# Optimization experiments

Measured on AMD Instinct MI355X. Metric: run time of the kernel, lower is better.

The kernel has to match this reference:

```python
import jax, jax.numpy as jnp
import numpy as np


def setup_inputs() -> dict:
    key = jax.random.key(0)
    k1, k2 = jax.random.split(key)
    b, t_x, d = 16, 1024, 256
    max_dur = 8
    x = jax.random.normal(k1, (b, t_x, d), dtype=jnp.float32)
    repeat_count = jax.random.randint(k2, (b, t_x), 0, max_dur, dtype=jnp.int64)
    out_len = t_x * (max_dur - 1)  # static upper bound on max(cumsum(durations))
    return {"x": x, "repeat_count": repeat_count, "out_len": out_len}


def reference(x, repeat_count, out_len):
    # x: (b, t_x, d); repeat_count: (b, t_x) int; out_len: static int (t_y)
    cum = jnp.cumsum(repeat_count.astype(jnp.int64), axis=1)          # (b, t_x)
    # content mask: M[b, i, j] = 1 if j < cum[b, i]
    cols = jnp.arange(out_len)                                        # (t_y,)
    M = (cols[None, None, :] < cum[:, :, None]).astype(x.dtype)       # (b, t_x, t_y)
    # row-wise diff along t_x turns prefix masks into per-phoneme one-hot spans
    M = jnp.concatenate([M[:, :1, :], M[:, 1:, :] - M[:, :-1, :]], axis=1)
    # bmm(M^T, x): expand phonemes into frames
    out = jnp.einsum('bxt,bxd->btd', M, x)                            # (b, t_y, d)
    lengths = jnp.max(cum, axis=1)                                    # (b,)
    return out, lengths
```

## Files before the change

kernel.cpp:

```cpp
#include <hip/hip_runtime.h>

#define B       16
#define TX      1024
#define D       256
#define OUT_LEN 7168
#define TILE    16

__global__ __launch_bounds__(256) void lr_scan_kernel(
        const int* __restrict__ rc,
        int* __restrict__ cum,
        float* __restrict__ len_out)
{
    __shared__ int part[256];
    const int b = blockIdx.x;
    const int t = threadIdx.x;

    const int4* rc4 = (const int4*)(rc + b * TX);
    int4 v = rc4[t];
    const int s0 = v.x;
    const int s1 = s0 + v.y;
    const int s2 = s1 + v.z;
    const int s3 = s2 + v.w;

    part[t] = s3;
    __syncthreads();

    #pragma unroll
    for (int off = 1; off < 256; off <<= 1) {
        int tmp = (t >= off) ? part[t - off] : 0;
        __syncthreads();
        part[t] += tmp;
        __syncthreads();
    }

    const int excl = part[t] - s3;
    int4 c;
    c.x = excl + s0;
    c.y = excl + s1;
    c.z = excl + s2;
    c.w = excl + s3;
    ((int4*)(cum + b * TX))[t] = c;

    if (t == 255) {
        len_out[b] = (float)part[255];
    }
}

__global__ __launch_bounds__(256) void lr_expand_kernel(
        const float* __restrict__ x,
        const int* __restrict__ cum,
        float* __restrict__ out)
{
    __shared__ int scum[TX];

    const int blocks_per_batch = OUT_LEN / TILE;
    const int b    = blockIdx.x / blocks_per_batch;
    const int row0 = (blockIdx.x % blocks_per_batch) * TILE;
    const int t    = threadIdx.x;

    ((int4*)scum)[t] = ((const int4*)(cum + b * TX))[t];
    __syncthreads();

    const int total = scum[TX - 1];
    const int lane4 = t & 63;
    const int sub   = t >> 6;

    const float4* x4   = (const float4*)(x + (size_t)b * TX * D);
    float4*       out4 = (float4*)(out + (size_t)b * OUT_LEN * D);

    #pragma unroll
    for (int r = sub; r < TILE; r += 4) {
        const int j = row0 + r;
        float4 val = make_float4(0.f, 0.f, 0.f, 0.f);
        if (j < total) {
            int i = 0;
            #pragma unroll
            for (int step = TX / 2; step > 0; step >>= 1) {
                if (scum[i + step - 1] <= j) i += step;
            }
            val = x4[(size_t)i * (D / 4) + lane4];
        }
        out4[(size_t)j * (D / 4) + lane4] = val;
    }
}

extern "C" void kernel_launch(void* const* d_in, const int* in_sizes, int n_in,
                              void* d_out, int out_size, void* d_ws, size_t ws_size,
                              hipStream_t stream) {
    const float* x  = (const float*)d_in[0];
    const int*   rc = (const int*)d_in[1];
    float* out = (float*)d_out;
    float* len_out = out + (size_t)B * OUT_LEN * D;
    int* cum = (int*)d_ws;

    lr_scan_kernel<<<B, 256, 0, stream>>>(rc, cum, len_out);

    const int grid = B * (OUT_LEN / TILE);
    lr_expand_kernel<<<grid, 256, 0, stream>>>(x, cum, out);
}
```

Baseline: 137.8 us.

## Precompute per-frame source index in scan kernel, replace binary search with gather

The scan kernel now writes a per-output-frame source phoneme index (or -1 for padding) directly, scattering spans, instead of writing the cumulative sums. The expand kernel drops the shared-memory cum load and per-row binary search, becoming a flat gather-copy where each thread handles four strided float4 elements. This removes the per-block shared load, the barrier and the search work. In exchange, the scan kernel runs serial span-filling loops on only 16 blocks, and the cross-batch flattened indexing relies on x and the source indices being laid out globally.

```diff
diff --git a/kernel.cpp b/kernel.cpp
--- a/kernel.cpp
+++ b/kernel.cpp
@@ -4,11 +4,12 @@
 #define TX      1024
 #define D       256
 #define OUT_LEN 7168
-#define TILE    16
+#define F4_PER_ROW (D / 4)
+#define TOTAL_F4 (B * OUT_LEN * F4_PER_ROW)
 
-__global__ __launch_bounds__(256) void lr_scan_kernel(
+__global__ __launch_bounds__(256) void lr_scan_src_kernel(
         const int* __restrict__ rc,
-        int* __restrict__ cum,
+        int* __restrict__ src,
         float* __restrict__ len_out)
 {
     __shared__ int part[256];
@@ -34,53 +35,46 @@
     }
 
     const int excl = part[t] - s3;
-    int4 c;
-    c.x = excl + s0;
-    c.y = excl + s1;
-    c.z = excl + s2;
-    c.w = excl + s3;
-    ((int4*)(cum + b * TX))[t] = c;
+    const int total = part[255];
+
+    int* srow = src + b * OUT_LEN;
+    const int gbase = b * TX + 4 * t;
+    int st[5];
+    st[0] = excl;
+    st[1] = excl + s0;
+    st[2] = excl + s1;
+    st[3] = excl + s2;
+    st[4] = excl + s3;
+    #pragma unroll
+    for (int k = 0; k < 4; k++) {
+        const int g = gbase + k;
+        for (int j = st[k]; j < st[k + 1]; j++) srow[j] = g;
+    }
+
+    for (int j = total + t; j < OUT_LEN; j += 256) srow[j] = -1;
 
     if (t == 255) {
-        len_out[b] = (float)part[255];
+        len_out[b] = (float)total;
     }
 }
 
 __global__ __launch_bounds__(256) void lr_expand_kernel(
-        const float* __restrict__ x,
-        const int* __restrict__ cum,
-        float* __restrict__ out)
+        const float4* __restrict__ x4,
+        const int* __restrict__ src,
+        float4* __restrict__ out4)
 {
-    __shared__ int scum[TX];
-
-    const int blocks_per_batch = OUT_LEN / TILE;
-    const int b    = blockIdx.x / blocks_per_batch;
-    const int row0 = (blockIdx.x % blocks_per_batch) * TILE;
-    const int t    = threadIdx.x;
-
-    ((int4*)scum)[t] = ((const int4*)(cum + b * TX))[t];
-    __syncthreads();
-
-    const int total = scum[TX - 1];
-    const int lane4 = t & 63;
-    const int sub   = t >> 6;
-
-    const float4* x4   = (const float4*)(x + (size_t)b * TX * D);
-    float4*       out4 = (float4*)(out + (size_t)b * OUT_LEN * D);
+    const int e0 = blockIdx.x * 256 + threadIdx.x;
+    const int stride = TOTAL_F4 / 4;
 
     #pragma unroll
-    for (int r = sub; r < TILE; r += 4) {
-        const int j = row0 + r;
+    for (int k = 0; k < 4; k++) {
+        const int e = e0 + k * stride;
+        const int s = src[e >> 6];
         float4 val = make_float4(0.f, 0.f, 0.f, 0.f);
-        if (j < total) {
-            int i = 0;
-            #pragma unroll
-            for (int step = TX / 2; step > 0; step >>= 1) {
-                if (scum[i + step - 1] <= j) i += step;
-            }
-            val = x4[(size_t)i * (D / 4) + lane4];
+        if (s >= 0) {
+            val = x4[((size_t)s << 6) | (e & 63)];
         }
-        out4[(size_t)j * (D / 4) + lane4] = val;
+        out4[e] = val;
     }
 }
 
@@ -91,10 +85,11 @@
     const int*   rc = (const int*)d_in[1];
     float* out = (float*)d_out;
     float* len_out = out + (size_t)B * OUT_LEN * D;
-    int* cum = (int*)d_ws;
+    int* src = (int*)d_ws;
 
-    lr_scan_kernel<<<B, 256, 0, stream>>>(rc, cum, len_out);
+    lr_scan_src_kernel<<<B, 256, 0, stream>>>(rc, src, len_out);
 
-    const int grid = B * (OUT_LEN / TILE);
-    lr_expand_kernel<<<grid, 256, 0, stream>>>(x, cum, out);
+    const int grid = TOTAL_F4 / (256 * 4);
+    lr_expand_kernel<<<grid, 256, 0, stream>>>(
+        (const float4*)x, src, (float4*)out);
 }
```

New measurement: 139.9 us. Within noise of the previous version (+1.5%).
